# Kernel tuning notes

Measured on AMD Instinct MI355X. Metric: run time of the kernel, lower is better.

## Reference

```python
import jax, jax.numpy as jnp
from jax import lax
import numpy as np

GRID = (1, 1, 4096, 4096)  # N, C, H, W
KSHAPE = (1, 1, 3, 3)      # O, I, kH, kW


def setup_inputs() -> dict:
    key = jax.random.key(0)
    k0, k1, k2 = jax.random.split(key, 3)
    r0 = jax.random.normal(k0, GRID, dtype=jnp.float32)
    p = jax.random.normal(k1, GRID, dtype=jnp.float32)
    phi = jnp.zeros(GRID, dtype=jnp.float32)
    filter = jax.random.normal(k2, KSHAPE, dtype=jnp.float32)
    return {"r0": r0, "p": p, "phi": phi, "filter": filter}


def reference(r0, p, phi, filter):
    # 3x3 stencil conv with padding=1 (same spatial size)
    conv_out = lax.conv_general_dilated(
        p, filter,
        window_strides=(1, 1),
        padding=[(1, 1), (1, 1)],
        dimension_numbers=("NCHW", "OIHW", "NCHW"),
    )
    rr0 = jnp.sum(r0 * r0)
    alpha = rr0 / jnp.sum(p * conv_out)
    r1 = r0 - alpha * conv_out
    phi_new = phi + alpha * p
    r1_sum = jnp.sum(r1 * r1)
    beta = r1_sum / rr0
    p_new = r1 + beta * p
    return (r1, p_new, phi_new, r1_sum)
```

## Files before the change

### kernel.cpp

```cpp
#include <hip/hip_runtime.h>

constexpr int H = 4096;
constexpr int W = 4096;
constexpr int NPIX = H * W;
constexpr int W4   = W / 4;
constexpr int NUNIT = 4 * H;
constexpr int K1_BLOCKS = 2048;
constexpr int K1_UNITS  = NUNIT / K1_BLOCKS;

typedef float f32x4 __attribute__((ext_vector_type(4)));

__device__ __forceinline__ void waveRed4(float& a, float& b, float& c, float& d) {
    #pragma unroll
    for (int o = 32; o > 0; o >>= 1) {
        a += __shfl_down(a, o, 64);
        b += __shfl_down(b, o, 64);
        c += __shfl_down(c, o, 64);
        d += __shfl_down(d, o, 64);
    }
}

__device__ __forceinline__ float4 rowconv(float l, float4 c, float r, float f0, float f1, float f2) {
    float4 o;
    o.x = f0 * l   + f1 * c.x + f2 * c.y;
    o.y = f0 * c.x + f1 * c.y + f2 * c.z;
    o.z = f0 * c.y + f1 * c.z + f2 * c.w;
    o.w = f0 * c.z + f1 * c.w + f2 * r;
    return o;
}

__device__ __forceinline__ void conv_unit(const float* __restrict__ p,
                                          const float f[9], int u,
                                          float4& cv_out, float4& pc_out) {
    const int h  = u >> 2;
    const int w4 = ((u & 3) << 8) + threadIdx.x;
    const int w0 = w4 << 2;

    const float* __restrict__ rowc = p + (size_t)h * W;
    const float* __restrict__ rowm = p + (size_t)(h > 0     ? h - 1 : 0    ) * W;
    const float* __restrict__ rowp = p + (size_t)(h < H - 1 ? h + 1 : H - 1) * W;
    const float mM = (h > 0)     ? 1.f : 0.f;
    const float pM = (h < H - 1) ? 1.f : 0.f;

    const float4 cm  = reinterpret_cast<const float4*>(rowm)[w4];
    const float4 cc4 = reinterpret_cast<const float4*>(rowc)[w4];
    const float4 cp  = reinterpret_cast<const float4*>(rowp)[w4];
    const int li = (w0 > 0) ? w0 - 1 : 0;
    const int ri = (w0 + 4 < W) ? w0 + 4 : W - 1;
    float lm = rowm[li], lc = rowc[li], lp = rowp[li];
    float rm = rowm[ri], rc = rowc[ri], rp = rowp[ri];

    const float lM = (w0 > 0) ? 1.f : 0.f;
    const float rM = (w0 + 4 < W) ? 1.f : 0.f;
    lm *= lM; lc *= lM; lp *= lM;
    rm *= rM; rc *= rM; rp *= rM;

    float4 cv = rowconv(lc, cc4, rc, f[3], f[4], f[5]);
    const float4 tm = rowconv(lm, cm, rm, f[0], f[1], f[2]);
    const float4 tp = rowconv(lp, cp, rp, f[6], f[7], f[8]);
    cv.x = fmaf(mM, tm.x, fmaf(pM, tp.x, cv.x));
    cv.y = fmaf(mM, tm.y, fmaf(pM, tp.y, cv.y));
    cv.z = fmaf(mM, tm.z, fmaf(pM, tp.z, cv.z));
    cv.w = fmaf(mM, tm.w, fmaf(pM, tp.w, cv.w));

    cv_out = cv;
    pc_out = cc4;
}

__global__ __launch_bounds__(256) void k1_sums(const float* __restrict__ r0,
                                               const float* __restrict__ p,
                                               const float* __restrict__ filt,
                                               float* __restrict__ partials) {
    __shared__ float sred[4][4];
    float f[9];
    #pragma unroll
    for (int i = 0; i < 9; ++i) f[i] = filt[i];

    const int lane = threadIdx.x & 63;
    const int wid  = threadIdx.x >> 6;

    float s0 = 0.f, s1 = 0.f, s2 = 0.f, s3 = 0.f;
    const int u0 = blockIdx.x * K1_UNITS;
    #pragma unroll 4
    for (int i = 0; i < K1_UNITS; ++i) {
        const int u = u0 + i;
        const int h  = u >> 2;
        const int w4 = ((u & 3) << 8) + threadIdx.x;
        float4 cv, pc;
        conv_unit(p, f, u, cv, pc);
        const float4 rv = reinterpret_cast<const float4*>(r0 + (size_t)h * W)[w4];
        s0 += rv.x*rv.x + rv.y*rv.y + rv.z*rv.z + rv.w*rv.w;
        s1 += pc.x*cv.x + pc.y*cv.y + pc.z*cv.z + pc.w*cv.w;
        s2 += rv.x*cv.x + rv.y*cv.y + rv.z*cv.z + rv.w*cv.w;
        s3 += cv.x*cv.x + cv.y*cv.y + cv.z*cv.z + cv.w*cv.w;
    }
    waveRed4(s0, s1, s2, s3);
    if (lane == 0) { sred[wid][0] = s0; sred[wid][1] = s1; sred[wid][2] = s2; sred[wid][3] = s3; }
    __syncthreads();
    if (threadIdx.x == 0) {
        f32x4 pv;
        pv.x = sred[0][0] + sred[1][0] + sred[2][0] + sred[3][0];
        pv.y = sred[0][1] + sred[1][1] + sred[2][1] + sred[3][1];
        pv.z = sred[0][2] + sred[1][2] + sred[2][2] + sred[3][2];
        pv.w = sred[0][3] + sred[1][3] + sred[2][3] + sred[3][3];
        reinterpret_cast<f32x4*>(partials)[blockIdx.x] = pv;
    }
}

__global__ __launch_bounds__(1024) void k_reduce(const float* __restrict__ partials,
                                                 float* __restrict__ scalars) {
    __shared__ float sred[16][4];
    const int lane = threadIdx.x & 63;
    const int wid  = threadIdx.x >> 6;

    f32x4 acc = reinterpret_cast<const f32x4*>(partials)[threadIdx.x]
              + reinterpret_cast<const f32x4*>(partials)[threadIdx.x + 1024];
    float s0 = acc.x, s1 = acc.y, s2 = acc.z, s3 = acc.w;
    waveRed4(s0, s1, s2, s3);
    if (lane == 0) { sred[wid][0] = s0; sred[wid][1] = s1; sred[wid][2] = s2; sred[wid][3] = s3; }
    __syncthreads();
    if (threadIdx.x == 0) {
        float rr0 = 0.f, pap = 0.f, r0c = 0.f, cc = 0.f;
        #pragma unroll
        for (int wv = 0; wv < 16; ++wv) {
            rr0 += sred[wv][0]; pap += sred[wv][1];
            r0c += sred[wv][2]; cc  += sred[wv][3];
        }
        const float alpha = rr0 / pap;
        const float r1s   = rr0 - 2.f * alpha * r0c + alpha * alpha * cc;
        scalars[0] = alpha;
        scalars[1] = r1s / rr0;
        scalars[2] = r1s;
    }
}

__global__ __launch_bounds__(256) void k2_update(const float* __restrict__ r0,
                                                 const float* __restrict__ p,
                                                 const float* __restrict__ phi,
                                                 const float* __restrict__ filt,
                                                 const float* __restrict__ scalars,
                                                 float* __restrict__ out) {
    const int b = blockIdx.x;
    const int h = b >> 2;
    const int w4 = ((b & 3) << 8) + threadIdx.x;
    const size_t vv = (size_t)h * W4 + w4;

    const float alpha = scalars[0];
    const float beta  = scalars[1];

    float f[9];
    #pragma unroll
    for (int i = 0; i < 9; ++i) f[i] = filt[i];

    float4 cv, pc;
    conv_unit(p, f, b, cv, pc);
    const float4 rv = reinterpret_cast<const float4*>(r0 + (size_t)h * W)[w4];
    const f32x4 ph = __builtin_nontemporal_load(
        reinterpret_cast<const f32x4*>(phi) + vv);

    f32x4 r1;
    r1.x = fmaf(-alpha, cv.x, rv.x);
    r1.y = fmaf(-alpha, cv.y, rv.y);
    r1.z = fmaf(-alpha, cv.z, rv.z);
    r1.w = fmaf(-alpha, cv.w, rv.w);
    f32x4 pn;
    pn.x = fmaf(beta, pc.x, r1.x);
    pn.y = fmaf(beta, pc.y, r1.y);
    pn.z = fmaf(beta, pc.z, r1.z);
    pn.w = fmaf(beta, pc.w, r1.w);
    f32x4 pho;
    pho.x = fmaf(alpha, pc.x, ph.x);
    pho.y = fmaf(alpha, pc.y, ph.y);
    pho.z = fmaf(alpha, pc.z, ph.z);
    pho.w = fmaf(alpha, pc.w, ph.w);

    f32x4* __restrict__ r1_out  = reinterpret_cast<f32x4*>(out);
    f32x4* __restrict__ pn_out  = reinterpret_cast<f32x4*>(out + (size_t)NPIX);
    f32x4* __restrict__ phi_out = reinterpret_cast<f32x4*>(out + 2 * (size_t)NPIX);
    __builtin_nontemporal_store(r1,  r1_out  + vv);
    __builtin_nontemporal_store(pn,  pn_out  + vv);
    __builtin_nontemporal_store(pho, phi_out + vv);

    if (b == 0 && threadIdx.x == 0) out[3 * (size_t)NPIX] = scalars[2];
}

extern "C" void kernel_launch(void* const* d_in, const int* in_sizes, int n_in,
                              void* d_out, int out_size, void* d_ws, size_t ws_size,
                              hipStream_t stream) {
    const float* r0   = (const float*)d_in[0];
    const float* p    = (const float*)d_in[1];
    const float* phi  = (const float*)d_in[2];
    const float* filt = (const float*)d_in[3];
    float* out      = (float*)d_out;
    float* partials = (float*)d_ws;
    float* scalars  = partials + 4 * K1_BLOCKS;

    hipLaunchKernelGGL(k1_sums,  dim3(K1_BLOCKS), dim3(256),  0, stream, r0, p, filt, partials);
    hipLaunchKernelGGL(k_reduce, dim3(1),         dim3(1024), 0, stream, partials, scalars);
    hipLaunchKernelGGL(k2_update,dim3(NUNIT),     dim3(256),  0, stream, r0, p, phi, filt, scalars, out);
}
```

Baseline: 124.6 us.

## Fuse reduction and update into one persistent kernel with a grid barrier

Replaces the three launches (partial sums, single-block reduce, update) with one persistent kernel of 1024 blocks. An atomic-counter grid barrier separates the reduction phase from the update phase, and every block redundantly reduces the 1024 partials to get alpha and beta. The aim is to remove launch gaps and the serial single-block reduce, and to re-read p and r0 while they may still be in cache. The cost is a memset launch, a spin barrier that relies on all 1024 blocks being resident at once, and less parallelism per phase. The phi load also drops its nontemporal hint.

```diff
diff --git a/kernel.cpp b/kernel.cpp
--- a/kernel.cpp
+++ b/kernel.cpp
@@ -5,8 +5,8 @@
 constexpr int NPIX = H * W;
 constexpr int W4   = W / 4;
 constexpr int NUNIT = 4 * H;
-constexpr int K1_BLOCKS = 2048;
-constexpr int K1_UNITS  = NUNIT / K1_BLOCKS;
+constexpr int GRID_B = 1024;
+constexpr int UNITS  = NUNIT / GRID_B;
 
 typedef float f32x4 __attribute__((ext_vector_type(4)));
 
@@ -67,22 +67,40 @@
     pc_out = cc4;
 }
 
-__global__ __launch_bounds__(256) void k1_sums(const float* __restrict__ r0,
-                                               const float* __restrict__ p,
-                                               const float* __restrict__ filt,
-                                               float* __restrict__ partials) {
+__device__ __forceinline__ void grid_barrier(unsigned* __restrict__ cnt) {
+    __syncthreads();
+    if (threadIdx.x == 0) {
+        __threadfence();
+        __hip_atomic_fetch_add(cnt, 1u, __ATOMIC_RELEASE, __HIP_MEMORY_SCOPE_AGENT);
+        int guard = 0;
+        while (__hip_atomic_load(cnt, __ATOMIC_RELAXED, __HIP_MEMORY_SCOPE_AGENT) < (unsigned)GRID_B
+               && ++guard < (1 << 28)) { __builtin_amdgcn_s_sleep(8); }
+        (void)__hip_atomic_load(cnt, __ATOMIC_ACQUIRE, __HIP_MEMORY_SCOPE_AGENT);
+    }
+    __syncthreads();
+}
+
+__global__ __launch_bounds__(256) void cg_fused(const float* __restrict__ r0,
+                                                const float* __restrict__ p,
+                                                const float* __restrict__ phi,
+                                                const float* __restrict__ filt,
+                                                float* __restrict__ out,
+                                                float* __restrict__ partials,
+                                                unsigned* __restrict__ cnt) {
     __shared__ float sred[4][4];
+    __shared__ float sbc[4];
+
     float f[9];
     #pragma unroll
     for (int i = 0; i < 9; ++i) f[i] = filt[i];
 
     const int lane = threadIdx.x & 63;
     const int wid  = threadIdx.x >> 6;
+    const int u0   = blockIdx.x * UNITS;
 
     float s0 = 0.f, s1 = 0.f, s2 = 0.f, s3 = 0.f;
-    const int u0 = blockIdx.x * K1_UNITS;
-    #pragma unroll 4
-    for (int i = 0; i < K1_UNITS; ++i) {
+    #pragma unroll 2
+    for (int i = 0; i < UNITS; ++i) {
         const int u = u0 + i;
         const int h  = u >> 2;
         const int w4 = ((u & 3) << 8) + threadIdx.x;
@@ -105,83 +123,66 @@
         pv.w = sred[0][3] + sred[1][3] + sred[2][3] + sred[3][3];
         reinterpret_cast<f32x4*>(partials)[blockIdx.x] = pv;
     }
-}
-
-__global__ __launch_bounds__(1024) void k_reduce(const float* __restrict__ partials,
-                                                 float* __restrict__ scalars) {
-    __shared__ float sred[16][4];
-    const int lane = threadIdx.x & 63;
-    const int wid  = threadIdx.x >> 6;
-
-    f32x4 acc = reinterpret_cast<const f32x4*>(partials)[threadIdx.x]
-              + reinterpret_cast<const f32x4*>(partials)[threadIdx.x + 1024];
-    float s0 = acc.x, s1 = acc.y, s2 = acc.z, s3 = acc.w;
-    waveRed4(s0, s1, s2, s3);
-    if (lane == 0) { sred[wid][0] = s0; sred[wid][1] = s1; sred[wid][2] = s2; sred[wid][3] = s3; }
+
+    grid_barrier(cnt);
+
+    f32x4 acc = {0.f, 0.f, 0.f, 0.f};
+    #pragma unroll
+    for (int j = 0; j < GRID_B / 256; ++j)
+        acc += reinterpret_cast<const f32x4*>(partials)[threadIdx.x + 256 * j];
+    float b0 = acc.x, b1 = acc.y, b2 = acc.z, b3 = acc.w;
+    waveRed4(b0, b1, b2, b3);
+    __syncthreads();
+    if (lane == 0) { sred[wid][0] = b0; sred[wid][1] = b1; sred[wid][2] = b2; sred[wid][3] = b3; }
     __syncthreads();
     if (threadIdx.x == 0) {
-        float rr0 = 0.f, pap = 0.f, r0c = 0.f, cc = 0.f;
-        #pragma unroll
-        for (int wv = 0; wv < 16; ++wv) {
-            rr0 += sred[wv][0]; pap += sred[wv][1];
-            r0c += sred[wv][2]; cc  += sred[wv][3];
-        }
+        const float rr0 = sred[0][0] + sred[1][0] + sred[2][0] + sred[3][0];
+        const float pap = sred[0][1] + sred[1][1] + sred[2][1] + sred[3][1];
+        const float r0c = sred[0][2] + sred[1][2] + sred[2][2] + sred[3][2];
+        const float cc  = sred[0][3] + sred[1][3] + sred[2][3] + sred[3][3];
         const float alpha = rr0 / pap;
         const float r1s   = rr0 - 2.f * alpha * r0c + alpha * alpha * cc;
-        scalars[0] = alpha;
-        scalars[1] = r1s / rr0;
-        scalars[2] = r1s;
-    }
-}
-
-__global__ __launch_bounds__(256) void k2_update(const float* __restrict__ r0,
-                                                 const float* __restrict__ p,
-                                                 const float* __restrict__ phi,
-                                                 const float* __restrict__ filt,
-                                                 const float* __restrict__ scalars,
-                                                 float* __restrict__ out) {
-    const int b = blockIdx.x;
-    const int h = b >> 2;
-    const int w4 = ((b & 3) << 8) + threadIdx.x;
-    const size_t vv = (size_t)h * W4 + w4;
-
-    const float alpha = scalars[0];
-    const float beta  = scalars[1];
-
-    float f[9];
-    #pragma unroll
-    for (int i = 0; i < 9; ++i) f[i] = filt[i];
-
-    float4 cv, pc;
-    conv_unit(p, f, b, cv, pc);
-    const float4 rv = reinterpret_cast<const float4*>(r0 + (size_t)h * W)[w4];
-    const f32x4 ph = __builtin_nontemporal_load(
-        reinterpret_cast<const f32x4*>(phi) + vv);
-
-    f32x4 r1;
-    r1.x = fmaf(-alpha, cv.x, rv.x);
-    r1.y = fmaf(-alpha, cv.y, rv.y);
-    r1.z = fmaf(-alpha, cv.z, rv.z);
-    r1.w = fmaf(-alpha, cv.w, rv.w);
-    f32x4 pn;
-    pn.x = fmaf(beta, pc.x, r1.x);
-    pn.y = fmaf(beta, pc.y, r1.y);
-    pn.z = fmaf(beta, pc.z, r1.z);
-    pn.w = fmaf(beta, pc.w, r1.w);
-    f32x4 pho;
-    pho.x = fmaf(alpha, pc.x, ph.x);
-    pho.y = fmaf(alpha, pc.y, ph.y);
-    pho.z = fmaf(alpha, pc.z, ph.z);
-    pho.w = fmaf(alpha, pc.w, ph.w);
+        sbc[0] = alpha;
+        sbc[1] = r1s / rr0;
+        sbc[2] = r1s;
+    }
+    __syncthreads();
+    const float alpha = sbc[0];
+    const float beta  = sbc[1];
 
     f32x4* __restrict__ r1_out  = reinterpret_cast<f32x4*>(out);
     f32x4* __restrict__ pn_out  = reinterpret_cast<f32x4*>(out + (size_t)NPIX);
     f32x4* __restrict__ phi_out = reinterpret_cast<f32x4*>(out + 2 * (size_t)NPIX);
-    __builtin_nontemporal_store(r1,  r1_out  + vv);
-    __builtin_nontemporal_store(pn,  pn_out  + vv);
-    __builtin_nontemporal_store(pho, phi_out + vv);
-
-    if (b == 0 && threadIdx.x == 0) out[3 * (size_t)NPIX] = scalars[2];
+    #pragma unroll 2
+    for (int i = 0; i < UNITS; ++i) {
+        const int u = u0 + i;
+        const int h  = u >> 2;
+        const int w4 = ((u & 3) << 8) + threadIdx.x;
+        const size_t vv = (size_t)h * W4 + w4;
+        float4 cv, pc;
+        conv_unit(p, f, u, cv, pc);
+        const float4 rv = reinterpret_cast<const float4*>(r0 + (size_t)h * W)[w4];
+        const f32x4 ph = reinterpret_cast<const f32x4*>(phi)[vv];
+        f32x4 r1;
+        r1.x = fmaf(-alpha, cv.x, rv.x);
+        r1.y = fmaf(-alpha, cv.y, rv.y);
+        r1.z = fmaf(-alpha, cv.z, rv.z);
+        r1.w = fmaf(-alpha, cv.w, rv.w);
+        f32x4 pn;
+        pn.x = fmaf(beta, pc.x, r1.x);
+        pn.y = fmaf(beta, pc.y, r1.y);
+        pn.z = fmaf(beta, pc.z, r1.z);
+        pn.w = fmaf(beta, pc.w, r1.w);
+        f32x4 pho;
+        pho.x = fmaf(alpha, pc.x, ph.x);
+        pho.y = fmaf(alpha, pc.y, ph.y);
+        pho.z = fmaf(alpha, pc.z, ph.z);
+        pho.w = fmaf(alpha, pc.w, ph.w);
+        __builtin_nontemporal_store(r1,  r1_out  + vv);
+        __builtin_nontemporal_store(pn,  pn_out  + vv);
+        __builtin_nontemporal_store(pho, phi_out + vv);
+    }
+    if (blockIdx.x == 0 && threadIdx.x == 0) out[3 * (size_t)NPIX] = sbc[2];
 }
 
 extern "C" void kernel_launch(void* const* d_in, const int* in_sizes, int n_in,
@@ -193,9 +194,10 @@
     const float* filt = (const float*)d_in[3];
     float* out      = (float*)d_out;
     float* partials = (float*)d_ws;
-    float* scalars  = partials + 4 * K1_BLOCKS;
-
-    hipLaunchKernelGGL(k1_sums,  dim3(K1_BLOCKS), dim3(256),  0, stream, r0, p, filt, partials);
-    hipLaunchKernelGGL(k_reduce, dim3(1),         dim3(1024), 0, stream, partials, scalars);
-    hipLaunchKernelGGL(k2_update,dim3(NUNIT),     dim3(256),  0, stream, r0, p, phi, filt, scalars, out);
-}
+    unsigned* cnt   = (unsigned*)((char*)d_ws + GRID_B * 16);
+
+    hipMemsetAsync(cnt, 0, sizeof(unsigned), stream);
+
+    hipLaunchKernelGGL(cg_fused, dim3(GRID_B), dim3(256), 0, stream,
+                       r0, p, phi, filt, out, partials, cnt);
+}
```

New measurement: 268.2 us. +115.2%, slower.

## Store conv result from first pass and fold final reduction into it

Applied to the files above, without the earlier changes.

The first kernel now writes the 3x3 stencil output into the p_new output slot. The second kernel reads it back instead of recomputing the convolution, streaming r0, p, phi and the stored conv with two float4 units per thread. The separate single-block reduce kernel is replaced by a last-block-done atomic ticket inside the first kernel, which needs a memset before each launch. This removes the stencil recompute and one launch, but adds a full-array write and read of the conv values to a pass that was already memory-bound.

```diff
diff --git a/kernel.cpp b/kernel.cpp
--- a/kernel.cpp
+++ b/kernel.cpp
@@ -7,6 +7,7 @@
 constexpr int NUNIT = 4 * H;
 constexpr int K1_BLOCKS = 2048;
 constexpr int K1_UNITS  = NUNIT / K1_BLOCKS;
+constexpr int K2_BLOCKS = 8192;
 
 typedef float f32x4 __attribute__((ext_vector_type(4)));
 
@@ -70,14 +71,20 @@
 __global__ __launch_bounds__(256) void k1_sums(const float* __restrict__ r0,
                                                const float* __restrict__ p,
                                                const float* __restrict__ filt,
-                                               float* __restrict__ partials) {
+                                               float* __restrict__ out,
+                                               float* __restrict__ partials,
+                                               float* __restrict__ scalars,
+                                               unsigned* __restrict__ ticket) {
     __shared__ float sred[4][4];
+    __shared__ int amLast;
     float f[9];
     #pragma unroll
     for (int i = 0; i < 9; ++i) f[i] = filt[i];
 
     const int lane = threadIdx.x & 63;
     const int wid  = threadIdx.x >> 6;
+
+    f32x4* __restrict__ cmid = reinterpret_cast<f32x4*>(out + (size_t)NPIX);
 
     float s0 = 0.f, s1 = 0.f, s2 = 0.f, s3 = 0.f;
     const int u0 = blockIdx.x * K1_UNITS;
@@ -86,9 +93,12 @@
         const int u = u0 + i;
         const int h  = u >> 2;
         const int w4 = ((u & 3) << 8) + threadIdx.x;
+        const size_t vv = (size_t)h * W4 + w4;
         float4 cv, pc;
         conv_unit(p, f, u, cv, pc);
         const float4 rv = reinterpret_cast<const float4*>(r0 + (size_t)h * W)[w4];
+        f32x4 cvv = { cv.x, cv.y, cv.z, cv.w };
+        cmid[vv] = cvv;
         s0 += rv.x*rv.x + rv.y*rv.y + rv.z*rv.z + rv.w*rv.w;
         s1 += pc.x*cv.x + pc.y*cv.y + pc.z*cv.z + pc.w*cv.w;
         s2 += rv.x*cv.x + rv.y*cv.y + rv.z*cv.z + rv.w*cv.w;
@@ -104,83 +114,79 @@
         pv.z = sred[0][2] + sred[1][2] + sred[2][2] + sred[3][2];
         pv.w = sred[0][3] + sred[1][3] + sred[2][3] + sred[3][3];
         reinterpret_cast<f32x4*>(partials)[blockIdx.x] = pv;
-    }
-}
-
-__global__ __launch_bounds__(1024) void k_reduce(const float* __restrict__ partials,
-                                                 float* __restrict__ scalars) {
-    __shared__ float sred[16][4];
-    const int lane = threadIdx.x & 63;
-    const int wid  = threadIdx.x >> 6;
-
-    f32x4 acc = reinterpret_cast<const f32x4*>(partials)[threadIdx.x]
-              + reinterpret_cast<const f32x4*>(partials)[threadIdx.x + 1024];
-    float s0 = acc.x, s1 = acc.y, s2 = acc.z, s3 = acc.w;
-    waveRed4(s0, s1, s2, s3);
-    if (lane == 0) { sred[wid][0] = s0; sred[wid][1] = s1; sred[wid][2] = s2; sred[wid][3] = s3; }
+        __threadfence();
+        const unsigned prev = __hip_atomic_fetch_add(ticket, 1u, __ATOMIC_ACQ_REL,
+                                                     __HIP_MEMORY_SCOPE_AGENT);
+        amLast = (prev == (unsigned)(K1_BLOCKS - 1));
+    }
     __syncthreads();
-    if (threadIdx.x == 0) {
-        float rr0 = 0.f, pap = 0.f, r0c = 0.f, cc = 0.f;
+
+    if (amLast) {
+        f32x4 acc = {0.f, 0.f, 0.f, 0.f};
         #pragma unroll
-        for (int wv = 0; wv < 16; ++wv) {
-            rr0 += sred[wv][0]; pap += sred[wv][1];
-            r0c += sred[wv][2]; cc  += sred[wv][3];
+        for (int j = 0; j < K1_BLOCKS / 256; ++j)
+            acc += reinterpret_cast<const f32x4*>(partials)[threadIdx.x + 256 * j];
+        float b0 = acc.x, b1 = acc.y, b2 = acc.z, b3 = acc.w;
+        waveRed4(b0, b1, b2, b3);
+        if (lane == 0) { sred[wid][0] = b0; sred[wid][1] = b1; sred[wid][2] = b2; sred[wid][3] = b3; }
+        __syncthreads();
+        if (threadIdx.x == 0) {
+            const float rr0 = sred[0][0] + sred[1][0] + sred[2][0] + sred[3][0];
+            const float pap = sred[0][1] + sred[1][1] + sred[2][1] + sred[3][1];
+            const float r0c = sred[0][2] + sred[1][2] + sred[2][2] + sred[3][2];
+            const float cc  = sred[0][3] + sred[1][3] + sred[2][3] + sred[3][3];
+            const float alpha = rr0 / pap;
+            const float r1s   = rr0 - 2.f * alpha * r0c + alpha * alpha * cc;
+            scalars[0] = alpha;
+            scalars[1] = r1s / rr0;
+            scalars[2] = r1s;
         }
-        const float alpha = rr0 / pap;
-        const float r1s   = rr0 - 2.f * alpha * r0c + alpha * alpha * cc;
-        scalars[0] = alpha;
-        scalars[1] = r1s / rr0;
-        scalars[2] = r1s;
     }
 }
 
 __global__ __launch_bounds__(256) void k2_update(const float* __restrict__ r0,
                                                  const float* __restrict__ p,
                                                  const float* __restrict__ phi,
-                                                 const float* __restrict__ filt,
                                                  const float* __restrict__ scalars,
                                                  float* __restrict__ out) {
-    const int b = blockIdx.x;
-    const int h = b >> 2;
-    const int w4 = ((b & 3) << 8) + threadIdx.x;
-    const size_t vv = (size_t)h * W4 + w4;
-
     const float alpha = scalars[0];
     const float beta  = scalars[1];
 
-    float f[9];
-    #pragma unroll
-    for (int i = 0; i < 9; ++i) f[i] = filt[i];
-
-    float4 cv, pc;
-    conv_unit(p, f, b, cv, pc);
-    const float4 rv = reinterpret_cast<const float4*>(r0 + (size_t)h * W)[w4];
-    const f32x4 ph = __builtin_nontemporal_load(
-        reinterpret_cast<const f32x4*>(phi) + vv);
-
-    f32x4 r1;
-    r1.x = fmaf(-alpha, cv.x, rv.x);
-    r1.y = fmaf(-alpha, cv.y, rv.y);
-    r1.z = fmaf(-alpha, cv.z, rv.z);
-    r1.w = fmaf(-alpha, cv.w, rv.w);
-    f32x4 pn;
-    pn.x = fmaf(beta, pc.x, r1.x);
-    pn.y = fmaf(beta, pc.y, r1.y);
-    pn.z = fmaf(beta, pc.z, r1.z);
-    pn.w = fmaf(beta, pc.w, r1.w);
-    f32x4 pho;
-    pho.x = fmaf(alpha, pc.x, ph.x);
-    pho.y = fmaf(alpha, pc.y, ph.y);
-    pho.z = fmaf(alpha, pc.z, ph.z);
-    pho.w = fmaf(alpha, pc.w, ph.w);
+    const int b = blockIdx.x;
+    const int h = b >> 1;
+    const int w4a = ((b & 1) << 9) + threadIdx.x;
+    const size_t base = (size_t)h * W4;
 
     f32x4* __restrict__ r1_out  = reinterpret_cast<f32x4*>(out);
     f32x4* __restrict__ pn_out  = reinterpret_cast<f32x4*>(out + (size_t)NPIX);
     f32x4* __restrict__ phi_out = reinterpret_cast<f32x4*>(out + 2 * (size_t)NPIX);
-    __builtin_nontemporal_store(r1,  r1_out  + vv);
-    __builtin_nontemporal_store(pn,  pn_out  + vv);
-    __builtin_nontemporal_store(pho, phi_out + vv);
-
+
+    #pragma unroll
+    for (int k = 0; k < 2; ++k) {
+        const size_t vv = base + w4a + 256 * k;
+        const f32x4 c  = __builtin_nontemporal_load(pn_out + vv);
+        const f32x4 rv = reinterpret_cast<const f32x4*>(r0)[vv];
+        const f32x4 pv = reinterpret_cast<const f32x4*>(p)[vv];
+        const f32x4 ph = reinterpret_cast<const f32x4*>(phi)[vv];
+        f32x4 r1;
+        r1.x = fmaf(-alpha, c.x, rv.x);
+        r1.y = fmaf(-alpha, c.y, rv.y);
+        r1.z = fmaf(-alpha, c.z, rv.z);
+        r1.w = fmaf(-alpha, c.w, rv.w);
+        f32x4 pn;
+        pn.x = fmaf(beta, pv.x, r1.x);
+        pn.y = fmaf(beta, pv.y, r1.y);
+        pn.z = fmaf(beta, pv.z, r1.z);
+        pn.w = fmaf(beta, pv.w, r1.w);
+        f32x4 pho;
+        pho.x = fmaf(alpha, pv.x, ph.x);
+        pho.y = fmaf(alpha, pv.y, ph.y);
+        pho.z = fmaf(alpha, pv.z, ph.z);
+        pho.w = fmaf(alpha, pv.w, ph.w);
+        __builtin_nontemporal_store(r1,  r1_out  + vv);
+        __builtin_nontemporal_store(pn,  pn_out  + vv);
+        __builtin_nontemporal_store(pho, phi_out + vv);
+    }
     if (b == 0 && threadIdx.x == 0) out[3 * (size_t)NPIX] = scalars[2];
 }
 
@@ -194,8 +200,12 @@
     float* out      = (float*)d_out;
     float* partials = (float*)d_ws;
     float* scalars  = partials + 4 * K1_BLOCKS;
-
-    hipLaunchKernelGGL(k1_sums,  dim3(K1_BLOCKS), dim3(256),  0, stream, r0, p, filt, partials);
-    hipLaunchKernelGGL(k_reduce, dim3(1),         dim3(1024), 0, stream, partials, scalars);
-    hipLaunchKernelGGL(k2_update,dim3(NUNIT),     dim3(256),  0, stream, r0, p, phi, filt, scalars, out);
-}
+    unsigned* ticket = (unsigned*)(scalars + 4);
+
+    hipMemsetAsync(ticket, 0, sizeof(unsigned), stream);
+
+    hipLaunchKernelGGL(k1_sums,  dim3(K1_BLOCKS), dim3(256), 0, stream,
+                       r0, p, filt, out, partials, scalars, ticket);
+    hipLaunchKernelGGL(k2_update, dim3(K2_BLOCKS), dim3(256), 0, stream,
+                       r0, p, phi, scalars, out);
+}
```

Measured after the change: 266.3 us. 114% more time.
